# Kernel optimization log

Measured on AMD Instinct MI355X. Metric: run time of the kernel, lower is better.

Reference implementation:

```python
import jax, jax.numpy as jnp
import numpy as np

DIM = 384
HEADS = 8
RED = 2
WS = 8            # window size for Q
DWS = WS // 2     # window size for DWT-downsampled K/V
DIM_Q = DIM // RED
HEAD_D = DIM_Q // HEADS
SCALE = HEAD_D ** -0.5
B, H, W = 4, 256, 256


def setup_inputs() -> dict:
    key = jax.random.key(0)
    ks = jax.random.split(key, 5)
    x = jax.random.normal(ks[0], (B, DIM, H, W), dtype=jnp.float32)
    q_w = jax.random.normal(ks[1], (DIM_Q, DIM), dtype=jnp.float32) * 0.02
    # grouped 1x1 conv: Conv2d(4*DIM, 2*DIM_Q, groups=4) -> (out=2*DIM_Q, in_per_group=DIM)
    kv_w = jax.random.normal(ks[2], (2 * DIM_Q, DIM), dtype=jnp.float32) * 0.02
    proj_w = jax.random.normal(ks[3], (DIM, DIM_Q), dtype=jnp.float32) * 0.02
    proj_b = jax.random.normal(ks[4], (DIM,), dtype=jnp.float32) * 0.02
    return {"x": x, "q_w": q_w, "kv_w": kv_w, "proj_w": proj_w, "proj_b": proj_b}


def _dwt2d(x):
    # Haar DWT via 2x2 stride-2 grouped conv; output channel 4c+s = subband s of input channel c
    b, c, h, w = x.shape
    xr = x.reshape(b, c, h // 2, 2, w // 2, 2)
    a = xr[:, :, :, 0, :, 0]
    bb = xr[:, :, :, 0, :, 1]
    cc = xr[:, :, :, 1, :, 0]
    dd = xr[:, :, :, 1, :, 1]
    ll = 0.5 * (a + bb + cc + dd)
    lh = 0.5 * (-a - bb + cc + dd)
    hl = 0.5 * (-a + bb - cc + dd)
    hh = 0.5 * (a - bb - cc + dd)
    sub = jnp.stack([ll, lh, hl, hh], axis=2)  # (b, c, 4, h/2, w/2)
    return sub.reshape(b, 4 * c, h // 2, w // 2)


def _to_windows(f, ws, heads):
    # f: (b, heads*d, h, w) -> (b*nH*nW, heads, ws*ws, d)
    b, cq, h, w = f.shape
    d = cq // heads
    t = f.reshape(b, heads, d, h // ws, ws, w // ws, ws)
    t = t.transpose(0, 3, 5, 1, 4, 6, 2)  # (b, nH, nW, heads, ws, ws, d)
    return t.reshape(b * (h // ws) * (w // ws), heads, ws * ws, d)


def reference(x, q_w, kv_w, proj_w, proj_b):
    b, c, h, w = x.shape
    # Q path: 1x1 conv bottleneck
    q_feat = jnp.einsum('oc,bchw->bohw', q_w, x)
    # K/V path: DWT then grouped (g=4) 1x1 conv
    xd = _dwt2d(x)                                   # (b, 4c, h/2, w/2)
    xd_g = xd.reshape(b, 4, c, h // 2, w // 2)
    kv_wg = kv_w.reshape(4, (2 * DIM_Q) // 4, c)
    kv = jnp.einsum('goc,bgchw->bgohw', kv_wg, xd_g).reshape(b, 2 * DIM_Q, h // 2, w // 2)
    k_feat, v_feat = kv[:, :DIM_Q], kv[:, DIM_Q:]
    # window partition
    qw = _to_windows(q_feat, WS, HEADS)              # (nw, h, 64, d)
    kw = _to_windows(k_feat, DWS, HEADS)             # (nw, h, 16, d)
    vw = _to_windows(v_feat, DWS, HEADS)
    corr = jnp.einsum('whqd,whkd->whqk', qw, kw) * SCALE   # no softmax
    attn = jnp.einsum('whqk,whkd->whqd', corr, vw)         # (nw, heads, 64, d)
    # merge windows back: (b*nH*nW, heads, ws*ws, d) -> (b, heads*d, H, W)
    nH, nW = h // WS, w // WS
    t = attn.reshape(b, nH, nW, HEADS, WS, WS, HEAD_D)
    t = t.transpose(0, 3, 6, 1, 4, 2, 5)             # (b, heads, d, nH, ws, nW, ws)
    feat = t.reshape(b, DIM_Q, h, w)
    out = jnp.einsum('oc,bchw->bohw', proj_w, feat) + proj_b[None, :, None, None]
    return out
```

## Files before the change

### kernel.cpp

```cpp
#include <hip/hip_runtime.h>

#define DIM    384
#define DIM_Q  192
#define HEADS  8
#define HEAD_D 24
#define BATCH  4
#define HH     256
#define WW     256
#define NWIN   32
#define SCALE  0.20412414523193154f

__global__ __launch_bounds__(256) void wave_attn_fused(
    const float* __restrict__ x, const float* __restrict__ q_w,
    const float* __restrict__ kv_w, const float* __restrict__ proj_w,
    const float* __restrict__ proj_b, float* __restrict__ out)
{
    __shared__ float qbuf[DIM_Q * 64];
    __shared__ float kvbuf[DIM * 16];
    __shared__ float xs[96 * 64];
    float* mbuf = xs;

    const int t   = threadIdx.x;
    const int blk = blockIdx.x;
    const int b   = blk >> 10;
    const int wy  = (blk >> 5) & 31;
    const int wx  = blk & 31;
    const int by  = wy * 8, bx = wx * 8;

    const int tx = t & 15;
    const int ty = t >> 4;

    const int i2 = (tx >> 2) * 2;
    const int j2 = (tx & 3) * 2;

    float4 accq[12];
#pragma unroll
    for (int i = 0; i < 12; ++i) accq[i] = make_float4(0.f, 0.f, 0.f, 0.f);

    for (int g = 0; g < 4; ++g) {
#pragma unroll
        for (int k = 0; k < 6; ++k) {
            int idx = t + (k << 8);
            int f  = idx & 1;
            int pi = (idx >> 1) & 7;
            int cl = idx >> 4;
            const float4 v = *(const float4*)(
                x + (((size_t)(b * DIM + g * 96 + cl) * HH + by + pi) * WW + bx + f * 4));
            *(float4*)&xs[cl * 64 + pi * 8 + f * 4] = v;
        }
        __syncthreads();

        for (int c4 = 0; c4 < 24; ++c4) {
            const float4 xv0 = *(const float4*)&xs[(c4 * 4 + 0) * 64 + tx * 4];
            const float4 xv1 = *(const float4*)&xs[(c4 * 4 + 1) * 64 + tx * 4];
            const float4 xv2 = *(const float4*)&xs[(c4 * 4 + 2) * 64 + tx * 4];
            const float4 xv3 = *(const float4*)&xs[(c4 * 4 + 3) * 64 + tx * 4];
#pragma unroll
            for (int i = 0; i < 12; ++i) {
                const float4 w = *(const float4*)(q_w + (ty + 16 * i) * DIM + g * 96 + c4 * 4);
                accq[i].x += w.x * xv0.x + w.y * xv1.x + w.z * xv2.x + w.w * xv3.x;
                accq[i].y += w.x * xv0.y + w.y * xv1.y + w.z * xv2.y + w.w * xv3.y;
                accq[i].z += w.x * xv0.z + w.y * xv1.z + w.z * xv2.z + w.w * xv3.z;
                accq[i].w += w.x * xv0.w + w.y * xv1.w + w.z * xv2.w + w.w * xv3.w;
            }
        }

        {
            float acck[6] = {0.f, 0.f, 0.f, 0.f, 0.f, 0.f};
            for (int cl = 0; cl < 96; ++cl) {
                const float a  = xs[cl * 64 + i2 * 8 + j2];
                const float bb = xs[cl * 64 + i2 * 8 + j2 + 1];
                const float cv = xs[cl * 64 + (i2 + 1) * 8 + j2];
                const float dv = xs[cl * 64 + (i2 + 1) * 8 + j2 + 1];
                const float ll = 0.5f * (a + bb + cv + dv);
                const float lh = 0.5f * (cv + dv - a - bb);
                const float hl = 0.5f * (bb + dv - a - cv);
                const float hh = 0.5f * (a + dv - bb - cv);
#pragma unroll
                for (int rr = 0; rr < 6; ++rr) {
                    const float4 w = *(const float4*)(kv_w + (g * 96 + ty * 6 + rr) * DIM + cl * 4);
                    acck[rr] += w.x * ll + w.y * lh + w.z * hl + w.w * hh;
                }
            }
#pragma unroll
            for (int rr = 0; rr < 6; ++rr)
                kvbuf[(g * 96 + ty * 6 + rr) * 16 + tx] = acck[rr];
        }
        __syncthreads();
    }

#pragma unroll
    for (int i = 0; i < 12; ++i)
        *(float4*)&qbuf[(ty + 16 * i) * 64 + tx * 4] = accq[i];

    if (t < DIM_Q) {
        const int h = t / 24, d1 = t % 24;
        float kvals[16];
#pragma unroll
        for (int p = 0; p < 16; ++p) kvals[p] = kvbuf[(h * 24 + d1) * 16 + p];
        for (int d2 = 0; d2 < 24; ++d2) {
            float s = 0.f;
#pragma unroll
            for (int p = 0; p < 16; ++p)
                s += kvals[p] * kvbuf[(DIM_Q + h * 24 + d2) * 16 + p];
            mbuf[(h * 24 + d1) * 24 + d2] = SCALE * s;
        }
    }
    __syncthreads();

    float4 featacc[12];
#pragma unroll
    for (int i = 0; i < 12; ++i) {
        const int ch = ty + 16 * i;
        const int h = ch / 24, d = ch % 24;
        float4 acc = make_float4(0.f, 0.f, 0.f, 0.f);
        for (int dp = 0; dp < 24; ++dp) {
            const float4 qv = *(const float4*)&qbuf[(h * 24 + dp) * 64 + tx * 4];
            const float m = mbuf[(h * 24 + dp) * 24 + d];
            acc.x += m * qv.x; acc.y += m * qv.y;
            acc.z += m * qv.z; acc.w += m * qv.w;
        }
        featacc[i] = acc;
    }
    __syncthreads();
#pragma unroll
    for (int i = 0; i < 12; ++i)
        *(float4*)&qbuf[(ty + 16 * i) * 64 + tx * 4] = featacc[i];
    __syncthreads();

    float4 acco[24];
#pragma unroll
    for (int i = 0; i < 24; ++i) acco[i] = make_float4(0.f, 0.f, 0.f, 0.f);
    for (int c4 = 0; c4 < 48; ++c4) {
        const float4 f0 = *(const float4*)&qbuf[(c4 * 4 + 0) * 64 + tx * 4];
        const float4 f1 = *(const float4*)&qbuf[(c4 * 4 + 1) * 64 + tx * 4];
        const float4 f2 = *(const float4*)&qbuf[(c4 * 4 + 2) * 64 + tx * 4];
        const float4 f3 = *(const float4*)&qbuf[(c4 * 4 + 3) * 64 + tx * 4];
#pragma unroll
        for (int i = 0; i < 24; ++i) {
            const float4 w = *(const float4*)(proj_w + (ty + 16 * i) * DIM_Q + c4 * 4);
            acco[i].x += w.x * f0.x + w.y * f1.x + w.z * f2.x + w.w * f3.x;
            acco[i].y += w.x * f0.y + w.y * f1.y + w.z * f2.y + w.w * f3.y;
            acco[i].z += w.x * f0.z + w.y * f1.z + w.z * f2.z + w.w * f3.z;
            acco[i].w += w.x * f0.w + w.y * f1.w + w.z * f2.w + w.w * f3.w;
        }
    }
    const int pi = tx >> 1;
    const int pj = (tx & 1) * 4;
#pragma unroll
    for (int i = 0; i < 24; ++i) {
        const int o = ty + 16 * i;
        const float bias = proj_b[o];
        float4 r = acco[i];
        r.x += bias; r.y += bias; r.z += bias; r.w += bias;
        *(float4*)(out + (((size_t)(b * DIM + o) * HH + by + pi) * WW + bx + pj)) = r;
    }
}

extern "C" void kernel_launch(void* const* d_in, const int* in_sizes, int n_in,
                              void* d_out, int out_size, void* d_ws, size_t ws_size,
                              hipStream_t stream) {
    const float* x      = (const float*)d_in[0];
    const float* q_w    = (const float*)d_in[1];
    const float* kv_w   = (const float*)d_in[2];
    const float* proj_w = (const float*)d_in[3];
    const float* proj_b = (const float*)d_in[4];
    float* out = (float*)d_out;
    (void)in_sizes; (void)n_in; (void)out_size; (void)d_ws; (void)ws_size;

    dim3 grid(BATCH * NWIN * NWIN);
    dim3 block(256);
    hipLaunchKernelGGL(wave_attn_fused, grid, block, 0, stream,
                       x, q_w, kv_w, proj_w, proj_b, out);
}
```

Before: 3.623 ms.

## Halve qbuf shared memory, pad kvbuf, swizzle blocks, target two blocks per CU

Processes the Q/attention/projection tail in two halves of 96 channels so qbuf shrinks from 192x64 to 96x64 floats, cutting LDS use. It also pads kvbuf rows to 17 to avoid bank conflicts, vectorises the DWT reads as float2, remaps block indices across batches, and requests two blocks per CU through launch bounds. The aim is higher occupancy and fewer LDS conflicts. In exchange it adds extra barriers and may cause register spills under the tighter register budget.

```diff
diff --git a/kernel.cpp b/kernel.cpp
--- a/kernel.cpp
+++ b/kernel.cpp
@@ -8,20 +8,21 @@
 #define HH     256
 #define WW     256
 #define NWIN   32
+#define KVP    17
 #define SCALE  0.20412414523193154f
 
-__global__ __launch_bounds__(256) void wave_attn_fused(
+__global__ __launch_bounds__(256, 2) void wave_attn_fused(
     const float* __restrict__ x, const float* __restrict__ q_w,
     const float* __restrict__ kv_w, const float* __restrict__ proj_w,
     const float* __restrict__ proj_b, float* __restrict__ out)
 {
-    __shared__ float qbuf[DIM_Q * 64];
-    __shared__ float kvbuf[DIM * 16];
+    __shared__ float qbuf[96 * 64];
+    __shared__ float kvbuf[DIM * KVP];
     __shared__ float xs[96 * 64];
     float* mbuf = xs;
 
-    const int t   = threadIdx.x;
-    const int blk = blockIdx.x;
+    const int t = threadIdx.x;
+    const int blk = ((int)blockIdx.x & 7) * 512 + ((int)blockIdx.x >> 3);
     const int b   = blk >> 10;
     const int wy  = (blk >> 5) & 31;
     const int wx  = blk & 31;
@@ -68,10 +69,10 @@
         {
             float acck[6] = {0.f, 0.f, 0.f, 0.f, 0.f, 0.f};
             for (int cl = 0; cl < 96; ++cl) {
-                const float a  = xs[cl * 64 + i2 * 8 + j2];
-                const float bb = xs[cl * 64 + i2 * 8 + j2 + 1];
-                const float cv = xs[cl * 64 + (i2 + 1) * 8 + j2];
-                const float dv = xs[cl * 64 + (i2 + 1) * 8 + j2 + 1];
+                const float2 ab = *(const float2*)&xs[cl * 64 + i2 * 8 + j2];
+                const float2 cd = *(const float2*)&xs[cl * 64 + (i2 + 1) * 8 + j2];
+                const float a  = ab.x, bb = ab.y;
+                const float cv = cd.x, dv = cd.y;
                 const float ll = 0.5f * (a + bb + cv + dv);
                 const float lh = 0.5f * (cv + dv - a - bb);
                 const float hl = 0.5f * (bb + dv - a - cv);
@@ -84,67 +85,75 @@
             }
 #pragma unroll
             for (int rr = 0; rr < 6; ++rr)
-                kvbuf[(g * 96 + ty * 6 + rr) * 16 + tx] = acck[rr];
+                kvbuf[(g * 96 + ty * 6 + rr) * KVP + tx] = acck[rr];
         }
         __syncthreads();
     }
-
-#pragma unroll
-    for (int i = 0; i < 12; ++i)
-        *(float4*)&qbuf[(ty + 16 * i) * 64 + tx * 4] = accq[i];
 
     if (t < DIM_Q) {
         const int h = t / 24, d1 = t % 24;
         float kvals[16];
 #pragma unroll
-        for (int p = 0; p < 16; ++p) kvals[p] = kvbuf[(h * 24 + d1) * 16 + p];
+        for (int p = 0; p < 16; ++p) kvals[p] = kvbuf[t * KVP + p];
         for (int d2 = 0; d2 < 24; ++d2) {
             float s = 0.f;
 #pragma unroll
             for (int p = 0; p < 16; ++p)
-                s += kvals[p] * kvbuf[(DIM_Q + h * 24 + d2) * 16 + p];
+                s += kvals[p] * kvbuf[(DIM_Q + h * 24 + d2) * KVP + p];
             mbuf[(h * 24 + d1) * 24 + d2] = SCALE * s;
         }
     }
     __syncthreads();
 
-    float4 featacc[12];
-#pragma unroll
-    for (int i = 0; i < 12; ++i) {
-        const int ch = ty + 16 * i;
-        const int h = ch / 24, d = ch % 24;
-        float4 acc = make_float4(0.f, 0.f, 0.f, 0.f);
-        for (int dp = 0; dp < 24; ++dp) {
-            const float4 qv = *(const float4*)&qbuf[(h * 24 + dp) * 64 + tx * 4];
-            const float m = mbuf[(h * 24 + dp) * 24 + d];
-            acc.x += m * qv.x; acc.y += m * qv.y;
-            acc.z += m * qv.z; acc.w += m * qv.w;
-        }
-        featacc[i] = acc;
-    }
-    __syncthreads();
-#pragma unroll
-    for (int i = 0; i < 12; ++i)
-        *(float4*)&qbuf[(ty + 16 * i) * 64 + tx * 4] = featacc[i];
-    __syncthreads();
-
     float4 acco[24];
 #pragma unroll
     for (int i = 0; i < 24; ++i) acco[i] = make_float4(0.f, 0.f, 0.f, 0.f);
-    for (int c4 = 0; c4 < 48; ++c4) {
-        const float4 f0 = *(const float4*)&qbuf[(c4 * 4 + 0) * 64 + tx * 4];
-        const float4 f1 = *(const float4*)&qbuf[(c4 * 4 + 1) * 64 + tx * 4];
-        const float4 f2 = *(const float4*)&qbuf[(c4 * 4 + 2) * 64 + tx * 4];
-        const float4 f3 = *(const float4*)&qbuf[(c4 * 4 + 3) * 64 + tx * 4];
+
 #pragma unroll
-        for (int i = 0; i < 24; ++i) {
-            const float4 w = *(const float4*)(proj_w + (ty + 16 * i) * DIM_Q + c4 * 4);
-            acco[i].x += w.x * f0.x + w.y * f1.x + w.z * f2.x + w.w * f3.x;
-            acco[i].y += w.x * f0.y + w.y * f1.y + w.z * f2.y + w.w * f3.y;
-            acco[i].z += w.x * f0.z + w.y * f1.z + w.z * f2.z + w.w * f3.z;
-            acco[i].w += w.x * f0.w + w.y * f1.w + w.z * f2.w + w.w * f3.w;
+    for (int r = 0; r < 2; ++r) {
+#pragma unroll
+        for (int ii = 0; ii < 6; ++ii)
+            *(float4*)&qbuf[(ty + 16 * ii) * 64 + tx * 4] = accq[ii + 6 * r];
+        __syncthreads();
+
+        float4 featacc[6];
+#pragma unroll
+        for (int ii = 0; ii < 6; ++ii) {
+            const int ch = 96 * r + ty + 16 * ii;
+            const int h  = ch / 24, d = ch % 24;
+            const int hl = (h - 4 * r) * 24;
+            float4 acc = make_float4(0.f, 0.f, 0.f, 0.f);
+            for (int dp = 0; dp < 24; ++dp) {
+                const float4 qv = *(const float4*)&qbuf[(hl + dp) * 64 + tx * 4];
+                const float m = mbuf[(h * 24 + dp) * 24 + d];
+                acc.x += m * qv.x; acc.y += m * qv.y;
+                acc.z += m * qv.z; acc.w += m * qv.w;
+            }
+            featacc[ii] = acc;
         }
+        __syncthreads();
+#pragma unroll
+        for (int ii = 0; ii < 6; ++ii)
+            *(float4*)&qbuf[(ty + 16 * ii) * 64 + tx * 4] = featacc[ii];
+        __syncthreads();
+
+        for (int c4 = 0; c4 < 24; ++c4) {
+            const float4 f0 = *(const float4*)&qbuf[(c4 * 4 + 0) * 64 + tx * 4];
+            const float4 f1 = *(const float4*)&qbuf[(c4 * 4 + 1) * 64 + tx * 4];
+            const float4 f2 = *(const float4*)&qbuf[(c4 * 4 + 2) * 64 + tx * 4];
+            const float4 f3 = *(const float4*)&qbuf[(c4 * 4 + 3) * 64 + tx * 4];
+#pragma unroll
+            for (int i = 0; i < 24; ++i) {
+                const float4 w = *(const float4*)(proj_w + (ty + 16 * i) * DIM_Q + 96 * r + c4 * 4);
+                acco[i].x += w.x * f0.x + w.y * f1.x + w.z * f2.x + w.w * f3.x;
+                acco[i].y += w.x * f0.y + w.y * f1.y + w.z * f2.y + w.w * f3.y;
+                acco[i].z += w.x * f0.z + w.y * f1.z + w.z * f2.z + w.w * f3.z;
+                acco[i].w += w.x * f0.w + w.y * f1.w + w.z * f2.w + w.w * f3.w;
+            }
+        }
+        __syncthreads();
     }
+
     const int pi = tx >> 1;
     const int pj = (tx & 1) * 4;
 #pragma unroll
```

Result: slower. 5.097 ms (+40.7%).
